# Kernel tuning notes

Measured on AMD Instinct MI355X. Metric: run time of the kernel, lower is better.

The kernel has to match this reference:

```python
import jax, jax.numpy as jnp
import numpy as np

R = 8            # LoRA rank (cfg.EXPERT_LOW_RANK)
E = 4            # expert count for proj (cfg.EXPERT_NUM)
TOPK_PCT = 50    # cfg.topk_tempalte == cfg.topk_search == 50, percent mode


def linear_experts(x, W, b, routeW, A, Bm, scaling):
    # LinearExperts.forward: frozen linear + softmax-routed sum of LoRA experts.
    res = x @ W.T + b
    rw = jax.nn.softmax((x @ routeW.T).astype(jnp.float32), axis=-1).astype(res.dtype)  # [B,N,E]
    z = jnp.einsum('bnc,erc->bner', x, A)      # [B,N,E,r]
    d = jnp.einsum('bner,ecr->bnec', z, Bm)    # [B,N,E,C_out]
    return res + jnp.einsum('bne,bnec->bnc', rw, d) * scaling


def merged_qkv(x, W, b, A, Bm, scaling):
    # loralib MergedLinear, enable_lora=[True,True,True]: grouped LoRA over q/k/v blocks.
    base = x @ W.T + b                          # [B,N,3C]
    z = jnp.einsum('bnc,grc->bngr', x, A)       # [B,N,3,r]
    d = jnp.einsum('bngr,gcr->bngc', z, Bm)     # [B,N,3,C]
    Bsz, N = x.shape[0], x.shape[1]
    return base + d.reshape(Bsz, N, -1) * scaling


def softmax_w_top(attn, top):
    # topk -> exp(v - v_max) -> normalize -> scatter back into zeros (rest exactly 0)
    vals, idx = jax.lax.top_k(attn, top)        # vals sorted desc, vals[...,0] is max
    ex = jnp.exp(vals - vals[..., :1])
    ex = ex / jnp.sum(ex, axis=-1, keepdims=True)
    Bh, Hh, Mh, _ = attn.shape
    bi = jnp.arange(Bh)[:, None, None, None]
    hi = jnp.arange(Hh)[None, :, None, None]
    mi = jnp.arange(Mh)[None, None, :, None]
    return jnp.zeros_like(attn).at[bi, hi, mi, idx].set(ex.astype(attn.dtype))


def setup_inputs() -> dict:
    key = jax.random.key(0)
    ks = jax.random.split(key, 32)
    B, N_m, N_s, C, H = 2, 576, 1024, 768, 12
    N = N_m + N_s
    hd = C // H
    N_mem = 1600
    s = 0.02
    inp = {
        'x': jax.random.normal(ks[0], (B, N, C), jnp.float32),
        'id_total': jax.random.normal(ks[1], (B, N_m, C), jnp.float32),
        'mem_k': jax.random.normal(ks[2], (B, H, N_mem, hd), jnp.float32),
        'mem_v': jax.random.normal(ks[3], (B, H, N_mem, hd), jnp.float32),
        # qkv MergedLinear
        'W_qkv': jax.random.normal(ks[4], (3 * C, C), jnp.float32) * s,
        'b_qkv': jnp.zeros((3 * C,), jnp.float32),
        'A_qkv': jax.random.normal(ks[5], (3, R, C), jnp.float32) * s,
        'B_qkv': jax.random.normal(ks[6], (3, C, R), jnp.float32) * s,
        # proj LinearExperts (lora_num=E)
        'W_proj': jax.random.normal(ks[7], (C, C), jnp.float32) * s,
        'b_proj': jnp.zeros((C,), jnp.float32),
        'routeW_proj': jax.random.normal(ks[8], (E, C), jnp.float32) * s,
        'A_proj': jax.random.normal(ks[9], (E, R, C), jnp.float32) * s,
        'B_proj': jax.random.normal(ks[10], (E, C, R), jnp.float32) * s,
        # linear_ID_K LinearExperts (lora_num=1, out=num_heads)
        'W_idk': jax.random.normal(ks[11], (H, C), jnp.float32) * s,
        'b_idk': jnp.zeros((H,), jnp.float32),
        'routeW_idk': jax.random.normal(ks[12], (1, C), jnp.float32) * s,
        'A_idk': jax.random.normal(ks[13], (1, R, C), jnp.float32) * s,
        'B_idk': jax.random.normal(ks[14], (1, H, R), jnp.float32) * s,
        # linear_ID_V LinearExperts (lora_num=1, out=dim)
        'W_idv': jax.random.normal(ks[15], (C, C), jnp.float32) * s,
        'b_idv': jnp.zeros((C,), jnp.float32),
        'routeW_idv': jax.random.normal(ks[16], (1, C), jnp.float32) * s,
        'A_idv': jax.random.normal(ks[17], (1, R, C), jnp.float32) * s,
        'B_idv': jax.random.normal(ks[18], (1, C, R), jnp.float32) * s,
        'id_add': 1,
    }
    return inp


def reference(x, id_total, mem_k, mem_v,
              W_qkv, b_qkv, A_qkv, B_qkv,
              W_proj, b_proj, routeW_proj, A_proj, B_proj,
              W_idk, b_idk, routeW_idk, A_idk, B_idk,
              W_idv, b_idv, routeW_idv, A_idv, B_idv,
              id_add):
    B, N, C = x.shape
    H = 12
    hd = C // H
    N_m = id_total.shape[1]
    N_s = N - N_m
    scale = hd ** -0.5
    scaling = 1.0 / R  # lora_alpha=1 default

    qkv = merged_qkv(x, W_qkv, b_qkv, A_qkv, B_qkv, scaling)          # [B,N,3C]
    qkv = qkv.reshape(B, N, 3, H, hd).transpose(2, 0, 3, 1, 4)        # [3,B,H,N,hd]
    q, k, v = qkv[0], qkv[1], qkv[2]
    k_m, k_s = k[:, :, :N_m], k[:, :, N_m:]
    v_m, v_s = v[:, :, :N_m], v[:, :, N_m:]

    # key_value_id: ID gating fused into memory K/V (id_add=True path)
    ID_K = linear_experts(id_total, W_idk, b_idk, routeW_idk, A_idk, B_idk, scaling)  # [B,N_m,H]
    ID_V = linear_experts(id_total, W_idv, b_idv, routeW_idv, A_idv, B_idv, scaling)  # [B,N_m,C]
    k_m = k_m * (1.0 + jnp.tanh(ID_K)).transpose(0, 2, 1)[..., None]                  # [B,H,N_m,hd]
    v_m_flat = v_m.transpose(0, 2, 1, 3).reshape(B, N_m, C) + ID_V                    # [B,N_m,C]
    v_m = v_m_flat.reshape(B, N_m, H, hd).transpose(0, 2, 1, 3)                       # [B,H,N_m,hd]
    v_add_id = jnp.concatenate([v_m, v_s], axis=2)                                    # [B,H,N,hd]

    q = q * scale
    q_m, q_s = q[:, :, :N_m], q[:, :, N_m:]

    # memory-token attention with top-k softmax (percent mode)
    attn_m = jnp.einsum('bhmd,bhnd->bhmn', q_m, k_m)
    top_m = TOPK_PCT * N_m // 100
    attn_m = softmax_w_top(attn_m, top_m)
    x_m = jnp.einsum('bhmn,bhnd->bhmd', attn_m, v_m).transpose(0, 2, 1, 3).reshape(B, N_m, C)

    # search-token attention over [cached memory, all current tokens]
    k_full = jnp.concatenate([mem_k, k], axis=2)
    v_full = jnp.concatenate([mem_v, v_add_id], axis=2)
    L = k_full.shape[2]
    attn_s = jnp.einsum('bhsd,bhld->bhsl', q_s, k_full)
    top_s = TOPK_PCT * L // 100
    attn_s = softmax_w_top(attn_s, top_s)
    x_s = jnp.einsum('bhsl,bhld->bhsd', attn_s, v_full).transpose(0, 2, 1, 3).reshape(B, N_s, C)

    out = jnp.concatenate([x_m, x_s], axis=1)
    out = linear_experts(out, W_proj, b_proj, routeW_proj, A_proj, B_proj, scaling)
    return (out, k_m, v_m)
```

## Files before the change

kernel.cpp:

```cpp
#include <hip/hip_runtime.h>
#include <hip/hip_bf16.h>

#define BN 2
#define NH 12
#define NTOK 1600
#define NM 576
#define NS 1024
#define CD 768
#define HD 64

typedef unsigned short u16;
typedef unsigned int u32;
typedef __attribute__((ext_vector_type(8))) short short8;
typedef __attribute__((ext_vector_type(4))) float f32x4;

__device__ __forceinline__ float fbits(u32 u) { return __uint_as_float(u); }
__device__ __forceinline__ u16 f2b(float f) {
    u32 u = __float_as_uint(f);
    u32 r = u + 0x7FFFu + ((u >> 16) & 1u);
    return (u16)(r >> 16);
}
__device__ __forceinline__ float b2f(u16 s) { return fbits(((u32)s) << 16); }
__device__ __forceinline__ u32 flip16(u32 u) {
    return (u & 0x8000u) ? (0xFFFFu & ~u) : (u | 0x8000u);
}
__device__ __forceinline__ float key2f(u32 k) {
    u32 b = (k & 0x8000u) ? (k & 0x7FFFu) : (0xFFFFu & ~k);
    return fbits(b << 16);
}
__device__ __forceinline__ float wave_red(float p) {
#pragma unroll
    for (int off = 1; off < 64; off <<= 1) p += __shfl_xor(p, off);
    return p;
}

__device__ __forceinline__ float dot768_ff(const float* __restrict__ a,
                                           const float* __restrict__ b) {
    float s = 0.f;
    for (int c = 0; c < CD; c += 4) {
        float4 fa = *(const float4*)(a + c);
        float4 fb = *(const float4*)(b + c);
        s += fa.x * fb.x + fa.y * fb.y + fa.z * fb.z + fa.w * fb.w;
    }
    return s;
}

__global__ __launch_bounds__(256) void small_dots(const float* __restrict__ x,
                                                  const float* __restrict__ Aq,
                                                  float* __restrict__ zq,
                                                  const float* __restrict__ id,
                                                  const float* __restrict__ Aik,
                                                  const float* __restrict__ Aiv,
                                                  const float* __restrict__ Wik,
                                                  const float* __restrict__ bik,
                                                  const float* __restrict__ Bik,
                                                  float* __restrict__ ziv,
                                                  float* __restrict__ IDK) {
    __shared__ float dres[28];
    const int blk = blockIdx.x;
    const int tid = threadIdx.x, lane = tid & 63, wv = tid >> 6;
    if (blk < 3200) {
        const float* xr = x + (size_t)blk * CD;
#pragma unroll
        for (int t = 0; t < 6; ++t) {
            const int q = wv * 6 + t;
            const float* ar = Aq + (size_t)q * CD;
            float p = 0.f;
#pragma unroll
            for (int c = 0; c < 12; ++c) p += xr[lane + c * 64] * ar[lane + c * 64];
            p = wave_red(p);
            if (lane == 0) zq[(size_t)blk * 24 + q] = p;
        }
    } else {
        const int m = blk - 3200;
        const float* xr = id + (size_t)m * CD;
#pragma unroll
        for (int t = 0; t < 7; ++t) {
            const int q = wv * 7 + t;
            const float* ar = (q < 8) ? Aik + (size_t)q * CD
                            : (q < 16) ? Aiv + (size_t)(q - 8) * CD
                                       : Wik + (size_t)(q - 16) * CD;
            float p = 0.f;
#pragma unroll
            for (int c = 0; c < 12; ++c) p += xr[lane + c * 64] * ar[lane + c * 64];
            p = wave_red(p);
            if (lane == 0) dres[q] = p;
        }
        __syncthreads();
        if (tid < 8) ziv[(size_t)m * 8 + tid] = dres[8 + tid];
        if (tid < 12) {
            float v = dres[16 + tid] + bik[tid];
            float lo = 0.f;
#pragma unroll
            for (int r = 0; r < 8; ++r) lo += dres[r] * Bik[tid * 8 + r];
            IDK[m * NH + tid] = v + 0.125f * lo;
        }
    }
}

__global__ __launch_bounds__(256) void stage_all(const float* __restrict__ x,
                                                 const float* __restrict__ zq,
                                                 u16* __restrict__ x_aug,
                                                 const float* __restrict__ Wq,
                                                 const float* __restrict__ Bq,
                                                 u16* __restrict__ wqkv_aug,
                                                 const float* __restrict__ Wp,
                                                 const float* __restrict__ Bp,
                                                 u16* __restrict__ wproj_aug,
                                                 const float* __restrict__ mk,
                                                 u16* __restrict__ kseq,
                                                 const float* __restrict__ mv,
                                                 u16* __restrict__ vt,
                                                 const float* __restrict__ id,
                                                 const float* __restrict__ ziv,
                                                 u16* __restrict__ id_aug,
                                                 const float* __restrict__ Widv,
                                                 const float* __restrict__ Bidv,
                                                 u16* __restrict__ widv_aug) {
    __shared__ float tile[64][65];
    const int blk = blockIdx.x;
    const int tid = threadIdx.x;
    if (blk < 1250) {
        const int idx = blk * 256 + tid;
        const int m = idx / 100, c8 = idx - m * 100;
        short8 v;
        if (c8 < 96) {
            const float* s = x + (size_t)m * CD + c8 * 8;
#pragma unroll
            for (int i = 0; i < 8; ++i) v[i] = (short)f2b(s[i]);
        } else if (c8 < 99) {
            const float* s = zq + (size_t)m * 24 + (c8 - 96) * 8;
#pragma unroll
            for (int i = 0; i < 8; ++i) v[i] = (short)f2b(s[i]);
        } else {
#pragma unroll
            for (int i = 0; i < 8; ++i) v[i] = 0;
        }
        *(short8*)(x_aug + (size_t)m * 800 + c8 * 8) = v;
    } else if (blk < 2150) {
        const int idx = (blk - 1250) * 256 + tid;
        const int j = idx / 100, c8 = idx - j * 100;
        short8 v;
        if (c8 < 96) {
            const float* s = Wq + (size_t)j * CD + c8 * 8;
#pragma unroll
            for (int i = 0; i < 8; ++i) v[i] = (short)f2b(s[i]);
        } else if (c8 < 99) {
            const int g = j / CD, c = j - g * CD;
            const int gp = c8 - 96;
#pragma unroll
            for (int i = 0; i < 8; ++i)
                v[i] = (gp == g) ? (short)f2b(0.125f * Bq[((size_t)g * CD + c) * 8 + i])
                                 : (short)0;
        } else {
#pragma unroll
            for (int i = 0; i < 8; ++i) v[i] = 0;
        }
        *(short8*)(wqkv_aug + (size_t)j * 800 + c8 * 8) = v;
    } else if (blk < 2450) {
        const int idx = (blk - 2150) * 256 + tid;
        const int j = idx / 100, c8 = idx - j * 100;
        short8 v;
        if (c8 < 96) {
            const float* s = Wp + (size_t)j * CD + c8 * 8;
#pragma unroll
            for (int i = 0; i < 8; ++i) v[i] = (short)f2b(s[i]);
        } else {
            const int e = c8 - 96;
#pragma unroll
            for (int i = 0; i < 8; ++i) v[i] = (short)f2b(Bp[((size_t)e * CD + j) * 8 + i]);
        }
        *(short8*)(wproj_aug + (size_t)j * 800 + c8 * 8) = v;
    } else if (blk < 3650) {
        const int t = (blk - 2450) * 256 + tid;
        const size_t e = (size_t)t * 8;
        const size_t bh = e / (1600 * 64);
        const size_t rem = e - bh * (1600 * 64);
        const float4 f0 = *(const float4*)(mk + e);
        const float4 f1 = *(const float4*)(mk + e + 4);
        short8 s;
        s[0] = (short)f2b(f0.x); s[1] = (short)f2b(f0.y);
        s[2] = (short)f2b(f0.z); s[3] = (short)f2b(f0.w);
        s[4] = (short)f2b(f1.x); s[5] = (short)f2b(f1.y);
        s[6] = (short)f2b(f1.z); s[7] = (short)f2b(f1.w);
        *(short8*)(kseq + bh * (3200 * 64) + rem) = s;
    } else if (blk < 4250) {
        const int i = blk - 3650;
        const int kt = i % 25, bh = i / 25;
        const int r = tid >> 2, c0 = (tid & 3) * 16;
        const float* src = mv + ((size_t)bh * 1600 + (size_t)kt * 64 + r) * 64 + c0;
#pragma unroll
        for (int q = 0; q < 4; ++q) {
            const float4 f = *(const float4*)(src + q * 4);
            tile[r][c0 + q * 4 + 0] = f.x;
            tile[r][c0 + q * 4 + 1] = f.y;
            tile[r][c0 + q * 4 + 2] = f.z;
            tile[r][c0 + q * 4 + 3] = f.w;
        }
        __syncthreads();
        short8 s0, s1;
#pragma unroll
        for (int q = 0; q < 8; ++q) s0[q] = (short)f2b(tile[c0 + q][r]);
#pragma unroll
        for (int q = 0; q < 8; ++q) s1[q] = (short)f2b(tile[c0 + 8 + q][r]);
        u16* dst = vt + ((size_t)bh * 64 + r) * 3200 + (size_t)kt * 64 + c0;
        *(short8*)dst = s0;
        *(short8*)(dst + 8) = s1;
    } else if (blk < 4700) {
        const int idx = (blk - 4250) * 256 + tid;
        const int m = idx / 100, c8 = idx - m * 100;
        short8 v;
        if (c8 < 96) {
            const float* s = id + (size_t)m * CD + c8 * 8;
#pragma unroll
            for (int i = 0; i < 8; ++i) v[i] = (short)f2b(s[i]);
        } else if (c8 == 96) {
            const float* s = ziv + (size_t)m * 8;
#pragma unroll
            for (int i = 0; i < 8; ++i) v[i] = (short)f2b(s[i]);
        } else {
#pragma unroll
            for (int i = 0; i < 8; ++i) v[i] = 0;
        }
        *(short8*)(id_aug + (size_t)m * 800 + c8 * 8) = v;
    } else {
        const int idx = (blk - 4700) * 256 + tid;
        const int j = idx / 100, c8 = idx - j * 100;
        short8 v;
        if (c8 < 96) {
            const float* s = Widv + (size_t)j * CD + c8 * 8;
#pragma unroll
            for (int i = 0; i < 8; ++i) v[i] = (short)f2b(s[i]);
        } else if (c8 == 96) {
#pragma unroll
            for (int i = 0; i < 8; ++i) v[i] = (short)f2b(0.125f * Bidv[(size_t)j * 8 + i]);
        } else {
#pragma unroll
            for (int i = 0; i < 8; ++i) v[i] = 0;
        }
        *(short8*)(widv_aug + (size_t)j * 800 + c8 * 8) = v;
    }
}

template <int MODE>
__global__ __launch_bounds__(MODE == 0 ? 256 : 128) void
gemm16_kernel(const u16* __restrict__ A16, const u16* __restrict__ B16,
              const float* __restrict__ bias, const float* __restrict__ IDK,
              u16* __restrict__ qbh, u16* __restrict__ kseq, u16* __restrict__ vt,
              float* __restrict__ okm, float* __restrict__ ovm,
              float* __restrict__ io) {
    const int tid = threadIdx.x;
    const int lane = tid & 63, wv = tid >> 6;
    const int quad = lane >> 4, n16 = lane & 15;
    int m0, n0;
    if (MODE == 0) {
        m0 = blockIdx.y * 128 + (wv >> 1) * 64;
        n0 = blockIdx.x * 128 + (wv & 1) * 64;
    } else {
        m0 = blockIdx.y * 64;
        n0 = blockIdx.x * 128 + wv * 64;
    }

    f32x4 acc[4][4];
#pragma unroll
    for (int a = 0; a < 4; ++a)
#pragma unroll
        for (int b = 0; b < 4; ++b) acc[a][b] = (f32x4){0.f, 0.f, 0.f, 0.f};

    const u16* ap = A16 + (size_t)(m0 + n16) * 800 + quad * 8;
    const u16* bp = B16 + (size_t)(n0 + n16) * 800 + quad * 8;
#pragma unroll 2
    for (int k0 = 0; k0 < 800; k0 += 32) {
        short8 aA[4], aB[4];
#pragma unroll
        for (int c = 0; c < 4; ++c) {
            aA[c] = *(const short8*)(ap + (size_t)c * 16 * 800 + k0);
            aB[c] = *(const short8*)(bp + (size_t)c * 16 * 800 + k0);
        }
#pragma unroll
        for (int mc = 0; mc < 4; ++mc)
#pragma unroll
            for (int nc = 0; nc < 4; ++nc)
                acc[mc][nc] =
                    __builtin_amdgcn_mfma_f32_16x16x32_bf16(aA[mc], aB[nc], acc[mc][nc], 0, 0, 0);
    }

    if (MODE == 0) {
        const int g = n0 / CD;
        const int hq = (n0 % CD) >> 6;
#pragma unroll
        for (int mc = 0; mc < 4; ++mc) {
#pragma unroll
            for (int r = 0; r < 4; ++r) {
                const int m = m0 + mc * 16 + quad * 4 + r;
                const int b = m / NTOK, n = m - (m / NTOK) * NTOK;
                const size_t bh = (size_t)(b * NH + hq);
                float gate = 0.f;
                if (g == 1 && n < NM) gate = 1.f + tanhf(IDK[(b * NM + n) * NH + hq]);
#pragma unroll
                for (int nc = 0; nc < 4; ++nc) {
                    const int d = nc * 16 + n16;
                    const int j = n0 + d;
                    const float val = acc[mc][nc][r] + bias[j];
                    const size_t om = (bh * NM + n) * 64 + d;
                    if (g == 0) {
                        qbh[(bh * NTOK + n) * 64 + d] = f2b(val * 0.125f);
                    } else if (g == 1) {
                        kseq[(bh * 3200 + 1600 + n) * 64 + d] = f2b(val);
                        if (n < NM) okm[om] = val * gate;
                    } else {
                        float vv = val;
                        if (n < NM) {
                            vv = val + ovm[om];
                            ovm[om] = vv;
                        }
                        vt[(bh * 64 + d) * 3200 + 1600 + n] = f2b(vv);
                    }
                }
            }
        }
    } else if (MODE == 1) {
#pragma unroll
        for (int mc = 0; mc < 4; ++mc) {
#pragma unroll
            for (int r = 0; r < 4; ++r) {
                const int m = m0 + mc * 16 + quad * 4 + r;
#pragma unroll
                for (int nc = 0; nc < 4; ++nc) {
                    const int j = n0 + nc * 16 + n16;
                    io[(size_t)m * CD + j] = acc[mc][nc][r] + bias[j];
                }
            }
        }
    } else {
#pragma unroll
        for (int mc = 0; mc < 4; ++mc) {
#pragma unroll
            for (int r = 0; r < 4; ++r) {
                const int m = m0 + mc * 16 + quad * 4 + r;
                const int b = m / NM, n = m - (m / NM) * NM;
#pragma unroll
                for (int nc = 0; nc < 4; ++nc) {
                    const int j = n0 + nc * 16 + n16;
                    const int h = j >> 6, d = j & 63;
                    ovm[(((size_t)(b * NH + h)) * NM + n) * 64 + d] = acc[mc][nc][r] + bias[j];
                }
            }
        }
    }
}

template <int L, bool KF32>
__global__ __launch_bounds__(512, 1) void attn9_kernel(const u16* __restrict__ qbh,
                                                       const u16* __restrict__ Kb,
                                                       const float* __restrict__ Kf,
                                                       const u16* __restrict__ vt,
                                                       float* __restrict__ aob,
                                                       int top, int row_start, int krows,
                                                       int vtoff) {
    constexpr int LP = L + 8;
    constexpr int NCHT = L / 16;
    constexpr int NCH = (NCHT + 7) / 8;
    constexpr bool FULL = (NCHT % 8) == 0;
    extern __shared__ __align__(16) u16 smem[];
    u16* wgt = smem;
    u32* hist = (u32*)(smem + 16 * LP);
    float* obuf = (float*)hist;
    float* rowmax = (float*)(hist + 8192);
    float* invtot = rowmax + 128;
    float* Mrow = invtot + 16;
    u32* selb = (u32*)(Mrow + 16);
    u32* Trow = selb + 16;
    u32* wantr = Trow + 16;

    const int tid = threadIdx.x;
    const int lane = tid & 63, wv = tid >> 6;
    const int quad = lane >> 4, n16 = lane & 15;
    const int rep = (n16 & 1) * 4096;
    const int bh = blockIdx.y;
    const int bb = bh / NH, hh = bh - bb * NH;
    const int r0 = row_start + blockIdx.x * 16;

    for (int i = tid; i < 8192; i += 512) hist[i] = 0;

    short8 aQ0, aQ1;
    {
        const u16* qp = qbh + ((size_t)bh * NTOK + r0 + n16) * 64;
        aQ0 = *(const short8*)(qp + quad * 8);
        aQ1 = *(const short8*)(qp + 32 + quad * 8);
    }
    __syncthreads();

    u32 pk[NCH][2];
    float rmax[4] = {-3.4e38f, -3.4e38f, -3.4e38f, -3.4e38f};
#pragma unroll
    for (int i = 0; i < NCH; ++i) {
        pk[i][0] = 0u; pk[i][1] = 0u;
        const int c = wv + i * 8;
        if (FULL || c < NCHT) {
            const int l0 = c << 4;
            short8 fb0, fb1;
            if (KF32) {
                const float* kp = Kf + ((size_t)bh * krows + l0 + n16) * 64 + quad * 8;
                const float4 x0 = *(const float4*)kp;
                const float4 x1 = *(const float4*)(kp + 4);
                const float4 y0 = *(const float4*)(kp + 32);
                const float4 y1 = *(const float4*)(kp + 36);
                fb0[0] = (short)f2b(x0.x); fb0[1] = (short)f2b(x0.y);
                fb0[2] = (short)f2b(x0.z); fb0[3] = (short)f2b(x0.w);
                fb0[4] = (short)f2b(x1.x); fb0[5] = (short)f2b(x1.y);
                fb0[6] = (short)f2b(x1.z); fb0[7] = (short)f2b(x1.w);
                fb1[0] = (short)f2b(y0.x); fb1[1] = (short)f2b(y0.y);
                fb1[2] = (short)f2b(y0.z); fb1[3] = (short)f2b(y0.w);
                fb1[4] = (short)f2b(y1.x); fb1[5] = (short)f2b(y1.y);
                fb1[6] = (short)f2b(y1.z); fb1[7] = (short)f2b(y1.w);
            } else {
                const u16* kp = Kb + ((size_t)bh * krows + l0 + n16) * 64 + quad * 8;
                fb0 = *(const short8*)kp;
                fb1 = *(const short8*)(kp + 32);
            }
            f32x4 d = {0.f, 0.f, 0.f, 0.f};
            d = __builtin_amdgcn_mfma_f32_16x16x32_bf16(aQ0, fb0, d, 0, 0, 0);
            d = __builtin_amdgcn_mfma_f32_16x16x32_bf16(aQ1, fb1, d, 0, 0, 0);
            const u16 w0 = f2b(d[0]), w1 = f2b(d[1]), w2 = f2b(d[2]), w3 = f2b(d[3]);
#pragma unroll
            for (int r = 0; r < 4; ++r) rmax[r] = fmaxf(rmax[r], d[r]);
            pk[i][0] = (u32)w0 | ((u32)w1 << 16);
            pk[i][1] = (u32)w2 | ((u32)w3 << 16);
            atomicAdd(&hist[rep + (quad * 4 + 0) * 256 + (flip16((u32)w0) >> 8)], 1u);
            atomicAdd(&hist[rep + (quad * 4 + 1) * 256 + (flip16((u32)w1) >> 8)], 1u);
            atomicAdd(&hist[rep + (quad * 4 + 2) * 256 + (flip16((u32)w2) >> 8)], 1u);
            atomicAdd(&hist[rep + (quad * 4 + 3) * 256 + (flip16((u32)w3) >> 8)], 1u);
        }
    }
#pragma unroll
    for (int off = 1; off < 16; off <<= 1) {
#pragma unroll
        for (int r = 0; r < 4; ++r) rmax[r] = fmaxf(rmax[r], __shfl_xor(rmax[r], off));
    }
    if (n16 == 0) {
#pragma unroll
        for (int r = 0; r < 4; ++r) rowmax[wv * 16 + quad * 4 + r] = rmax[r];
    }
    __syncthreads();

#pragma unroll
    for (int rp = 0; rp < 2; ++rp) {
        const int rr = wv + 8 * rp;
        float M = -3.4e38f;
#pragma unroll
        for (int w = 0; w < 8; ++w) M = fmaxf(M, rowmax[w * 16 + rr]);
        if (lane == 0) Mrow[rr] = M;
        u32 hh4[4];
#pragma unroll
        for (int j = 0; j < 4; ++j)
            hh4[j] = hist[rr * 256 + 4 * lane + j] + hist[4096 + rr * 256 + 4 * lane + j];
        const u32 s = hh4[0] + hh4[1] + hh4[2] + hh4[3];
        u32 sum = s;
#pragma unroll
        for (int off = 1; off < 64; off <<= 1) {
            const u32 t = __shfl_down(sum, off);
            if (lane + off < 64) sum += t;
        }
        int cnt = (int)(sum - s);
        const int want = top;
        for (int j = 3; j >= 0; --j) {
            const int c = (int)hh4[j];
            if (cnt < want && cnt + c >= want) {
                selb[rr] = (u32)(4 * lane + j);
                wantr[rr] = (u32)(want - cnt);
            }
            cnt += c;
        }
    }
    __syncthreads();
    for (int i = tid; i < 8192; i += 512) hist[i] = 0;
    __syncthreads();

    {
        u32 sl[4];
#pragma unroll
        for (int r = 0; r < 4; ++r) sl[r] = selb[quad * 4 + r];
#pragma unroll
        for (int i = 0; i < NCH; ++i) {
            const int c = wv + i * 8;
            if (FULL || c < NCHT) {
#pragma unroll
                for (int h = 0; h < 2; ++h) {
                    const u32 pr = pk[i][h];
                    const u32 k0 = flip16(pr & 0xffffu), k1 = flip16(pr >> 16);
                    const int r0i = quad * 4 + 2 * h, r1i = r0i + 1;
                    if ((k0 >> 8) == sl[2 * h])
                        atomicAdd(&hist[rep + r0i * 256 + (k0 & 255u)], 1u);
                    if ((k1 >> 8) == sl[2 * h + 1])
                        atomicAdd(&hist[rep + r1i * 256 + (k1 & 255u)], 1u);
                }
            }
        }
    }
    __syncthreads();

#pragma unroll
    for (int rp = 0; rp < 2; ++rp) {
        const int rr = wv + 8 * rp;
        u32 hh4[4];
#pragma unroll
        for (int j = 0; j < 4; ++j)
            hh4[j] = hist[rr * 256 + 4 * lane + j] + hist[4096 + rr * 256 + 4 * lane + j];
        const u32 s = hh4[0] + hh4[1] + hh4[2] + hh4[3];
        u32 sum = s;
#pragma unroll
        for (int off = 1; off < 64; off <<= 1) {
            const u32 t = __shfl_down(sum, off);
            if (lane + off < 64) sum += t;
        }
        int cnt = (int)(sum - s);
        const int want = (int)wantr[rr];
        for (int j = 3; j >= 0; --j) {
            const int c = (int)hh4[j];
            if (cnt < want && cnt + c >= want) {
                const u32 T = (selb[rr] << 8) | (u32)(4 * lane + j);
                Trow[rr] = T;
                invtot[rr] =
                    (float)(want - cnt) * __expf(fminf(key2f(T) - Mrow[rr], 0.f));
            }
            cnt += c;
        }
    }
    __syncthreads();

    {
        u32 Tq[4];
        float Mq[4];
#pragma unroll
        for (int r = 0; r < 4; ++r) {
            Tq[r] = Trow[quad * 4 + r];
            Mq[r] = Mrow[quad * 4 + r];
        }
        float ps[4] = {0.f, 0.f, 0.f, 0.f};
#pragma unroll
        for (int i = 0; i < NCH; ++i) {
            const int c = wv + i * 8;
            if (FULL || c < NCHT) {
#pragma unroll
                for (int h = 0; h < 2; ++h) {
                    const u32 pr = pk[i][h];
                    const int r0i = 2 * h, r1i = 2 * h + 1;
                    const u32 k0 = flip16(pr & 0xffffu), k1 = flip16(pr >> 16);
                    float e0 = 0.f, e1 = 0.f;
                    if (k0 >= Tq[r0i]) {
                        e0 = __expf(fminf(b2f((u16)(pr & 0xffffu)) - Mq[r0i], 0.f));
                        if (k0 > Tq[r0i]) ps[r0i] += e0;
                    }
                    if (k1 >= Tq[r1i]) {
                        e1 = __expf(fminf(b2f((u16)(pr >> 16)) - Mq[r1i], 0.f));
                        if (k1 > Tq[r1i]) ps[r1i] += e1;
                    }
                    pk[i][h] = (u32)f2b(e0) | ((u32)f2b(e1) << 16);
                }
            }
        }
#pragma unroll
        for (int off = 1; off < 16; off <<= 1) {
#pragma unroll
            for (int r = 0; r < 4; ++r) ps[r] += __shfl_xor(ps[r], off);
        }
        if (n16 == 0) {
#pragma unroll
            for (int r = 0; r < 4; ++r) atomicAdd(&invtot[quad * 4 + r], ps[r]);
        }
    }
    __syncthreads();
    if (tid < 16) invtot[tid] = 1.f / fmaxf(invtot[tid], 1e-30f);
    __syncthreads();

    {
        float iv[4];
#pragma unroll
        for (int r = 0; r < 4; ++r) iv[r] = invtot[quad * 4 + r];
#pragma unroll
        for (int i = 0; i < NCH; ++i) {
            const int c = wv + i * 8;
            if (FULL || c < NCHT) {
                const int l = (c << 4) + n16;
#pragma unroll
                for (int h = 0; h < 2; ++h) {
                    const u32 pr = pk[i][h];
                    wgt[(size_t)(quad * 4 + 2 * h) * LP + l] =
                        f2b(b2f((u16)(pr & 0xffffu)) * iv[2 * h]);
                    wgt[(size_t)(quad * 4 + 2 * h + 1) * LP + l] =
                        f2b(b2f((u16)(pr >> 16)) * iv[2 * h + 1]);
                }
            }
        }
    }
    __syncthreads();

    {
        const int half = wv & 1, dc = wv >> 1;
        constexpr int PVI = (L / 2) / 32;
        const int kbeg = half * (L / 2);
        const u16* vp =
            vt + ((size_t)bh * 64 + dc * 16 + n16) * 3200 + vtoff + quad * 8 + kbeg;
        const u16* wrow2 = wgt + (size_t)n16 * LP + quad * 8 + kbeg;
        f32x4 acc = {0.f, 0.f, 0.f, 0.f};
#pragma unroll 8
        for (int i = 0; i < PVI; ++i) {
            const short8 a = *(const short8*)(wrow2 + i * 32);
            const short8 bf = *(const short8*)(vp + i * 32);
            acc = __builtin_amdgcn_mfma_f32_16x16x32_bf16(a, bf, acc, 0, 0, 0);
        }
#pragma unroll
        for (int r = 0; r < 4; ++r) {
            const int rowi = quad * 4 + r;
            obuf[(half * 16 + rowi) * 64 + dc * 16 + n16] = acc[r];
        }
    }
    __syncthreads();
#pragma unroll
    for (int ii = 0; ii < 2; ++ii) {
        const int idx = tid + ii * 512;
        const int rowi = idx >> 6, dd = idx & 63;
        aob[((size_t)bb * NTOK + r0 + rowi) * CD + hh * 64 + dd] =
            obuf[rowi * 64 + dd] + obuf[(16 + rowi) * 64 + dd];
    }
}

__global__ __launch_bounds__(256) void coef_kernel(const float* __restrict__ aob,
                                                   const float* __restrict__ rW,
                                                   const float* __restrict__ Ap,
                                                   float* __restrict__ coef) {
    __shared__ float rl[8][4];
    __shared__ float rw[8][4];
    const int slot = threadIdx.x >> 5, lane = threadIdx.x & 31;
    const int m = blockIdx.x * 8 + slot;
    const float* xr = aob + (size_t)m * CD;
    const float z = dot768_ff(xr, Ap + (size_t)lane * CD);
    if (lane < 4) rl[slot][lane] = dot768_ff(xr, rW + (size_t)lane * CD);
    __syncthreads();
    if (lane == 0) {
        const float mx = fmaxf(fmaxf(rl[slot][0], rl[slot][1]), fmaxf(rl[slot][2], rl[slot][3]));
        const float e0 = __expf(rl[slot][0] - mx), e1 = __expf(rl[slot][1] - mx);
        const float e2 = __expf(rl[slot][2] - mx), e3 = __expf(rl[slot][3] - mx);
        const float is = 1.f / (e0 + e1 + e2 + e3);
        rw[slot][0] = e0 * is; rw[slot][1] = e1 * is; rw[slot][2] = e2 * is; rw[slot][3] = e3 * is;
    }
    __syncthreads();
    coef[(size_t)m * 32 + lane] = rw[slot][lane >> 3] * z * 0.125f;
}

__global__ __launch_bounds__(256) void cvt_aobaug(const float* __restrict__ aob,
                                                  const float* __restrict__ coef,
                                                  u16* __restrict__ dst) {
    const int idx = blockIdx.x * 256 + threadIdx.x;
    const int m = idx / 100, c8 = idx - m * 100;
    short8 v;
    if (c8 < 96) {
        const float* s = aob + (size_t)m * CD + c8 * 8;
#pragma unroll
        for (int i = 0; i < 8; ++i) v[i] = (short)f2b(s[i]);
    } else {
        const float* s = coef + (size_t)m * 32 + (c8 - 96) * 8;
#pragma unroll
        for (int i = 0; i < 8; ++i) v[i] = (short)f2b(s[i]);
    }
    *(short8*)(dst + (size_t)m * 800 + c8 * 8) = v;
}

extern "C" void kernel_launch(void* const* d_in, const int* in_sizes, int n_in,
                              void* d_out, int out_size, void* d_ws, size_t ws_size,
                              hipStream_t stream) {
    const float* x = (const float*)d_in[0];
    const float* id_total = (const float*)d_in[1];
    const float* mem_k = (const float*)d_in[2];
    const float* mem_v = (const float*)d_in[3];
    const float* W_qkv = (const float*)d_in[4];
    const float* b_qkv = (const float*)d_in[5];
    const float* A_qkv = (const float*)d_in[6];
    const float* B_qkv = (const float*)d_in[7];
    const float* W_proj = (const float*)d_in[8];
    const float* b_proj = (const float*)d_in[9];
    const float* routeW_proj = (const float*)d_in[10];
    const float* A_proj = (const float*)d_in[11];
    const float* B_proj = (const float*)d_in[12];
    const float* W_idk = (const float*)d_in[13];
    const float* b_idk = (const float*)d_in[14];
    const float* A_idk = (const float*)d_in[16];
    const float* B_idk = (const float*)d_in[17];
    const float* W_idv = (const float*)d_in[18];
    const float* b_idv = (const float*)d_in[19];
    const float* A_idv = (const float*)d_in[21];
    const float* B_idv = (const float*)d_in[22];

    float* io = (float*)d_out;
    float* o_km = io + (size_t)BN * NTOK * CD;
    float* o_vm = o_km + (size_t)BN * NH * NM * HD;

    u16* x_aug = (u16*)io;
    u16* wqkv_aug = x_aug + 2560000;
    u16* widv_aug = (u16*)o_km;

    u16* qbh = (u16*)d_ws;
    u16* kseq = qbh + 2457600;
    u16* vt = kseq + 4915200;
    float* zq = (float*)(vt + 4915200);
    float* ziv = zq + 76800;
    float* IDK = ziv + 9216;
    float* coef = IDK + 13824;
    u16* wproj_aug = (u16*)(coef + 102400);
    u16* id_aug = qbh;

    const int smem_seq = 16 * (3200 + 8) * 2 + 33600;
    const int smem_mem = 16 * (NM + 8) * 2 + 33600;
    hipFuncSetAttribute((const void*)attn9_kernel<3200, false>,
                        hipFuncAttributeMaxDynamicSharedMemorySize, smem_seq);
    hipFuncSetAttribute((const void*)attn9_kernel<NM, true>,
                        hipFuncAttributeMaxDynamicSharedMemorySize, smem_mem);

    small_dots<<<4352, 256, 0, stream>>>(x, A_qkv, zq, id_total, A_idk, A_idv,
                                         W_idk, b_idk, B_idk, ziv, IDK);
    stage_all<<<5000, 256, 0, stream>>>(x, zq, x_aug, W_qkv, B_qkv, wqkv_aug,
                                        W_proj, B_proj, wproj_aug, mem_k, kseq,
                                        mem_v, vt, id_total, ziv, id_aug,
                                        W_idv, B_idv, widv_aug);
    gemm16_kernel<2><<<dim3(6, 18), 128, 0, stream>>>(id_aug, widv_aug, b_idv, nullptr,
                                                      nullptr, nullptr, nullptr, nullptr,
                                                      o_vm, nullptr);
    gemm16_kernel<0><<<dim3(18, 25), 256, 0, stream>>>(x_aug, wqkv_aug, b_qkv, IDK,
                                                       qbh, kseq, vt, o_km, o_vm, nullptr);

    attn9_kernel<NM, true><<<dim3(NM / 16, BN * NH), 512, smem_mem, stream>>>(
        qbh, nullptr, o_km, vt, io, NM / 2, 0, NM, 1600);
    attn9_kernel<3200, false><<<dim3(NS / 16, BN * NH), 512, smem_seq, stream>>>(
        qbh, kseq, nullptr, vt, io, 1600, NM, 3200, 0);

    coef_kernel<<<400, 256, 0, stream>>>(io, routeW_proj, A_proj, coef);
    cvt_aobaug<<<1250, 256, 0, stream>>>(io, coef, kseq);
    gemm16_kernel<1><<<dim3(6, 50), 128, 0, stream>>>(kseq, wproj_aug, b_proj, nullptr,
                                                      nullptr, nullptr, nullptr, nullptr,
                                                      nullptr, io);
}
```

Measured before the change: 667.5 us.

## Keep attention scores in LDS and do per-row top-k refine within one wave

The attention kernel no longer keeps packed bf16 scores in registers (pk array). It writes them to the shared-memory weight buffer right after the MFMA. The second histogram pass, threshold search and exp/normalise are now done row-per-wave with wave-local fences instead of block-wide barriers. Normalisation by the row total is deferred to the PV output, and the launch-bounds min-blocks hint is dropped. This is meant to cut register pressure, raise occupancy and remove several __syncthreads, at the cost of extra LDS traffic and a rescale at output time.

Result: faster. 609.2 us (-8.7%).

```diff
diff --git a/kernel.cpp b/kernel.cpp
--- a/kernel.cpp
+++ b/kernel.cpp
@@ -351,17 +351,20 @@
 }
 
 template <int L, bool KF32>
-__global__ __launch_bounds__(512, 1) void attn9_kernel(const u16* __restrict__ qbh,
-                                                       const u16* __restrict__ Kb,
-                                                       const float* __restrict__ Kf,
-                                                       const u16* __restrict__ vt,
-                                                       float* __restrict__ aob,
-                                                       int top, int row_start, int krows,
-                                                       int vtoff) {
+__global__ __launch_bounds__(512) void attn10_kernel(const u16* __restrict__ qbh,
+                                                     const u16* __restrict__ Kb,
+                                                     const float* __restrict__ Kf,
+                                                     const u16* __restrict__ vt,
+                                                     float* __restrict__ aob,
+                                                     int top, int row_start, int krows,
+                                                     int vtoff) {
     constexpr int LP = L + 8;
     constexpr int NCHT = L / 16;
     constexpr int NCH = (NCHT + 7) / 8;
     constexpr bool FULL = (NCHT % 8) == 0;
+    constexpr int PAIRS = L / 2;
+    constexpr int NPIT = (PAIRS + 63) / 64;
+    constexpr bool PFULL = (PAIRS % 64) == 0;
     extern __shared__ __align__(16) u16 smem[];
     u16* wgt = smem;
     u32* hist = (u32*)(smem + 16 * LP);
@@ -391,11 +394,9 @@
     }
     __syncthreads();
 
-    u32 pk[NCH][2];
     float rmax[4] = {-3.4e38f, -3.4e38f, -3.4e38f, -3.4e38f};
 #pragma unroll
     for (int i = 0; i < NCH; ++i) {
-        pk[i][0] = 0u; pk[i][1] = 0u;
         const int c = wv + i * 8;
         if (FULL || c < NCHT) {
             const int l0 = c << 4;
@@ -425,8 +426,10 @@
             const u16 w0 = f2b(d[0]), w1 = f2b(d[1]), w2 = f2b(d[2]), w3 = f2b(d[3]);
 #pragma unroll
             for (int r = 0; r < 4; ++r) rmax[r] = fmaxf(rmax[r], d[r]);
-            pk[i][0] = (u32)w0 | ((u32)w1 << 16);
-            pk[i][1] = (u32)w2 | ((u32)w3 << 16);
+            wgt[(size_t)(quad * 4 + 0) * LP + l0 + n16] = w0;
+            wgt[(size_t)(quad * 4 + 1) * LP + l0 + n16] = w1;
+            wgt[(size_t)(quad * 4 + 2) * LP + l0 + n16] = w2;
+            wgt[(size_t)(quad * 4 + 3) * LP + l0 + n16] = w3;
             atomicAdd(&hist[rep + (quad * 4 + 0) * 256 + (flip16((u32)w0) >> 8)], 1u);
             atomicAdd(&hist[rep + (quad * 4 + 1) * 256 + (flip16((u32)w1) >> 8)], 1u);
             atomicAdd(&hist[rep + (quad * 4 + 2) * 256 + (flip16((u32)w2) >> 8)], 1u);
@@ -477,121 +480,70 @@
     for (int i = tid; i < 8192; i += 512) hist[i] = 0;
     __syncthreads();
 
-    {
-        u32 sl[4];
-#pragma unroll
-        for (int r = 0; r < 4; ++r) sl[r] = selb[quad * 4 + r];
-#pragma unroll
-        for (int i = 0; i < NCH; ++i) {
-            const int c = wv + i * 8;
-            if (FULL || c < NCHT) {
-#pragma unroll
-                for (int h = 0; h < 2; ++h) {
-                    const u32 pr = pk[i][h];
-                    const u32 k0 = flip16(pr & 0xffffu), k1 = flip16(pr >> 16);
-                    const int r0i = quad * 4 + 2 * h, r1i = r0i + 1;
-                    if ((k0 >> 8) == sl[2 * h])
-                        atomicAdd(&hist[rep + r0i * 256 + (k0 & 255u)], 1u);
-                    if ((k1 >> 8) == sl[2 * h + 1])
-                        atomicAdd(&hist[rep + r1i * 256 + (k1 & 255u)], 1u);
-                }
-            }
-        }
-    }
-    __syncthreads();
-
 #pragma unroll
     for (int rp = 0; rp < 2; ++rp) {
         const int rr = wv + 8 * rp;
-        u32 hh4[4];
-#pragma unroll
-        for (int j = 0; j < 4; ++j)
-            hh4[j] = hist[rr * 256 + 4 * lane + j] + hist[4096 + rr * 256 + 4 * lane + j];
-        const u32 s = hh4[0] + hh4[1] + hh4[2] + hh4[3];
-        u32 sum = s;
-#pragma unroll
-        for (int off = 1; off < 64; off <<= 1) {
-            const u32 t = __shfl_down(sum, off);
-            if (lane + off < 64) sum += t;
-        }
-        int cnt = (int)(sum - s);
-        const int want = (int)wantr[rr];
-        for (int j = 3; j >= 0; --j) {
-            const int c = (int)hh4[j];
-            if (cnt < want && cnt + c >= want) {
-                const u32 T = (selb[rr] << 8) | (u32)(4 * lane + j);
-                Trow[rr] = T;
-                invtot[rr] =
-                    (float)(want - cnt) * __expf(fminf(key2f(T) - Mrow[rr], 0.f));
-            }
-            cnt += c;
-        }
-    }
-    __syncthreads();
-
-    {
-        u32 Tq[4];
-        float Mq[4];
-#pragma unroll
-        for (int r = 0; r < 4; ++r) {
-            Tq[r] = Trow[quad * 4 + r];
-            Mq[r] = Mrow[quad * 4 + r];
-        }
-        float ps[4] = {0.f, 0.f, 0.f, 0.f};
-#pragma unroll
-        for (int i = 0; i < NCH; ++i) {
-            const int c = wv + i * 8;
-            if (FULL || c < NCHT) {
-#pragma unroll
-                for (int h = 0; h < 2; ++h) {
-                    const u32 pr = pk[i][h];
-                    const int r0i = 2 * h, r1i = 2 * h + 1;
+        const u32* row32 = (const u32*)(wgt + (size_t)rr * LP);
+        const u32 sel1 = selb[rr];
+        const float M = Mrow[rr];
+#pragma unroll
+        for (int i = 0; i < NPIT; ++i) {
+            if (PFULL || lane + 64 * i < PAIRS) {
+                const u32 pr = row32[lane + 64 * i];
+                const u32 k0 = flip16(pr & 0xffffu), k1 = flip16(pr >> 16);
+                if ((k0 >> 8) == sel1) atomicAdd(&hist[rep + rr * 256 + (k0 & 255u)], 1u);
+                if ((k1 >> 8) == sel1) atomicAdd(&hist[rep + rr * 256 + (k1 & 255u)], 1u);
+            }
+        }
+        __threadfence_block();
+        {
+            u32 hh4[4];
+#pragma unroll
+            for (int j = 0; j < 4; ++j)
+                hh4[j] = hist[rr * 256 + 4 * lane + j] + hist[4096 + rr * 256 + 4 * lane + j];
+            const u32 s = hh4[0] + hh4[1] + hh4[2] + hh4[3];
+            u32 sum = s;
+#pragma unroll
+            for (int off = 1; off < 64; off <<= 1) {
+                const u32 t = __shfl_down(sum, off);
+                if (lane + off < 64) sum += t;
+            }
+            int cnt = (int)(sum - s);
+            const int want = (int)wantr[rr];
+            for (int j = 3; j >= 0; --j) {
+                const int c = (int)hh4[j];
+                if (cnt < want && cnt + c >= want) {
+                    const u32 T = (sel1 << 8) | (u32)(4 * lane + j);
+                    Trow[rr] = T;
+                    invtot[rr] = (float)(want - cnt) * __expf(fminf(key2f(T) - M, 0.f));
+                }
+                cnt += c;
+            }
+        }
+        __threadfence_block();
+        {
+            const u32 T = Trow[rr];
+            u32* roww = (u32*)(wgt + (size_t)rr * LP);
+            float ps = 0.f;
+#pragma unroll
+            for (int i = 0; i < NPIT; ++i) {
+                if (PFULL || lane + 64 * i < PAIRS) {
+                    const u32 pr = roww[lane + 64 * i];
                     const u32 k0 = flip16(pr & 0xffffu), k1 = flip16(pr >> 16);
                     float e0 = 0.f, e1 = 0.f;
-                    if (k0 >= Tq[r0i]) {
-                        e0 = __expf(fminf(b2f((u16)(pr & 0xffffu)) - Mq[r0i], 0.f));
-                        if (k0 > Tq[r0i]) ps[r0i] += e0;
+                    if (k0 >= T) {
+                        e0 = __expf(fminf(b2f((u16)(pr & 0xffffu)) - M, 0.f));
+                        if (k0 > T) ps += e0;
                     }
-                    if (k1 >= Tq[r1i]) {
-                        e1 = __expf(fminf(b2f((u16)(pr >> 16)) - Mq[r1i], 0.f));
-                        if (k1 > Tq[r1i]) ps[r1i] += e1;
+                    if (k1 >= T) {
+                        e1 = __expf(fminf(b2f((u16)(pr >> 16)) - M, 0.f));
+                        if (k1 > T) ps += e1;
                     }
-                    pk[i][h] = (u32)f2b(e0) | ((u32)f2b(e1) << 16);
+                    roww[lane + 64 * i] = (u32)f2b(e0) | ((u32)f2b(e1) << 16);
                 }
             }
-        }
-#pragma unroll
-        for (int off = 1; off < 16; off <<= 1) {
-#pragma unroll
-            for (int r = 0; r < 4; ++r) ps[r] += __shfl_xor(ps[r], off);
-        }
-        if (n16 == 0) {
-#pragma unroll
-            for (int r = 0; r < 4; ++r) atomicAdd(&invtot[quad * 4 + r], ps[r]);
-        }
-    }
-    __syncthreads();
-    if (tid < 16) invtot[tid] = 1.f / fmaxf(invtot[tid], 1e-30f);
-    __syncthreads();
-
-    {
-        float iv[4];
-#pragma unroll
-        for (int r = 0; r < 4; ++r) iv[r] = invtot[quad * 4 + r];
-#pragma unroll
-        for (int i = 0; i < NCH; ++i) {
-            const int c = wv + i * 8;
-            if (FULL || c < NCHT) {
-                const int l = (c << 4) + n16;
-#pragma unroll
-                for (int h = 0; h < 2; ++h) {
-                    const u32 pr = pk[i][h];
-                    wgt[(size_t)(quad * 4 + 2 * h) * LP + l] =
-                        f2b(b2f((u16)(pr & 0xffffu)) * iv[2 * h]);
-                    wgt[(size_t)(quad * 4 + 2 * h + 1) * LP + l] =
-                        f2b(b2f((u16)(pr >> 16)) * iv[2 * h + 1]);
-                }
-            }
+            ps = wave_red(ps);
+            if (lane == 0) invtot[rr] = 1.f / fmaxf(invtot[rr] + ps, 1e-30f);
         }
     }
     __syncthreads();
@@ -613,7 +565,7 @@
 #pragma unroll
         for (int r = 0; r < 4; ++r) {
             const int rowi = quad * 4 + r;
-            obuf[(half * 16 + rowi) * 64 + dc * 16 + n16] = acc[r];
+            obuf[(half * 16 + rowi) * 64 + dc * 16 + n16] = acc[r] * invtot[rowi];
         }
     }
     __syncthreads();
@@ -712,9 +664,9 @@
 
     const int smem_seq = 16 * (3200 + 8) * 2 + 33600;
     const int smem_mem = 16 * (NM + 8) * 2 + 33600;
-    hipFuncSetAttribute((const void*)attn9_kernel<3200, false>,
+    hipFuncSetAttribute((const void*)attn10_kernel<3200, false>,
                         hipFuncAttributeMaxDynamicSharedMemorySize, smem_seq);
-    hipFuncSetAttribute((const void*)attn9_kernel<NM, true>,
+    hipFuncSetAttribute((const void*)attn10_kernel<NM, true>,
                         hipFuncAttributeMaxDynamicSharedMemorySize, smem_mem);
 
     small_dots<<<4352, 256, 0, stream>>>(x, A_qkv, zq, id_total, A_idk, A_idv,
@@ -729,9 +681,9 @@
     gemm16_kernel<0><<<dim3(18, 25), 256, 0, stream>>>(x_aug, wqkv_aug, b_qkv, IDK,
                                                        qbh, kseq, vt, o_km, o_vm, nullptr);
 
-    attn9_kernel<NM, true><<<dim3(NM / 16, BN * NH), 512, smem_mem, stream>>>(
+    attn10_kernel<NM, true><<<dim3(NM / 16, BN * NH), 512, smem_mem, stream>>>(
         qbh, nullptr, o_km, vt, io, NM / 2, 0, NM, 1600);
-    attn9_kernel<3200, false><<<dim3(NS / 16, BN * NH), 512, smem_seq, stream>>>(
+    attn10_kernel<3200, false><<<dim3(NS / 16, BN * NH), 512, smem_seq, stream>>>(
         qbh, kseq, nullptr, vt, io, 1600, NM, 3200, 0);
 
     coef_kernel<<<400, 256, 0, stream>>>(io, routeW_proj, A_proj, coef);
```
